# Kernel optimization log

Hardware: AMD Instinct MI355X
Metric: run time of the kernel (lower is better)

The kernel has to match this reference:

```python
import jax, jax.numpy as jnp
import numpy as np

# ---- static configuration (mirrors EarthSpecificBlock/EarthAttention3D) ----
WS = (2, 6, 12)                 # window_size (Z, H, W)
DIM = 192
HEADS = 6
DEPTH = 2
B, Z, H, W = 1, 8, 91, 180      # token grid entering the layer
PAD_H = (WS[1] - H % WS[1]) % WS[1]   # 5
PAD_W = (WS[2] - W % WS[2]) % WS[2]   # 0
HP, WP = H + PAD_H, W + PAD_W         # 96, 180
TOK = WS[0] * WS[1] * WS[2]           # 144 tokens per window
NZ, NH, NW = Z // WS[0], HP // WS[1], WP // WS[2]   # 4, 16, 15
TYPE_W = NZ * NH                      # 64 window types (Z x lat)
BIAS_ROWS = (2 * WS[2] - 1) * WS[1] * WS[1] * WS[0] * WS[0]  # 3312


def _construct_index():
    """Position index into the earth-specific bias table (EarthAttention3D._construct_index)."""
    zi = np.arange(WS[0]); zj = -np.arange(WS[0]) * WS[0]
    hi = np.arange(WS[1]); hj = -np.arange(WS[1]) * WS[1]
    w = np.arange(WS[2])
    c1 = np.stack(np.meshgrid(zi, hi, w, indexing='ij')).reshape(3, -1)
    c2 = np.stack(np.meshgrid(zj, hj, w, indexing='ij')).reshape(3, -1)
    coords = (c1[:, :, None] - c2[:, None, :]).transpose(1, 2, 0)
    coords[:, :, 2] += WS[2] - 1
    coords[:, :, 1] *= 2 * WS[2] - 1
    coords[:, :, 0] *= (2 * WS[2] - 1) * WS[1] * WS[1]
    return coords.sum(-1).reshape(-1)   # (TOK*TOK,)


def _gen_mask():
    """Shifted-window attention mask (gen_mask), shape (1, NW, TYPE_W, 1, TOK, TOK)."""
    m = np.zeros((1, Z, HP, WP, 1), np.float32)
    zs = (slice(0, -WS[0]), slice(-WS[0], -WS[0] // 2), slice(-WS[0] // 2, None))
    hs = (slice(0, -WS[1]), slice(-WS[1], -WS[1] // 2), slice(-WS[1] // 2, None))
    cnt = 0
    for zsl in zs:
        for hsl in hs:
            m[:, zsl, hsl, :, :] = cnt
            cnt += 1
    mw = m.reshape(1, NZ, WS[0], NH, WS[1], NW, WS[2], 1).transpose(0, 1, 3, 5, 2, 4, 6, 7)
    mw = mw.reshape(1, NZ, NH, NW, TOK)
    am = mw[:, :, :, :, None, :] - mw[:, :, :, :, :, None]
    am = np.where(am != 0, np.float32(-100.0), np.float32(0.0))
    return am.transpose(0, 3, 1, 2, 4, 5).reshape(1, NW, TYPE_W, 1, TOK, TOK)


POS_IDX = jnp.asarray(_construct_index())
MASK = jnp.asarray(_gen_mask())


def _ln(x, g, b):
    m = x.mean(-1, keepdims=True)
    v = ((x - m) ** 2).mean(-1, keepdims=True)
    return (x - m) * jax.lax.rsqrt(v + 1e-5) * g + b


def _block(x, qkv_w, qkv_b, proj_w, proj_b, bias_tab, g1, b1, g2, b2, w1, bm1, w2, bm2, roll):
    shortcut = x
    x = jnp.pad(x, ((0, 0), (0, 0), (0, PAD_H), (0, PAD_W), (0, 0)))
    if roll:
        x = jnp.roll(x, (-(WS[0] // 2), -(WS[1] // 2), -(WS[2] // 2)), axis=(1, 2, 3))
    # window partition: (B, NW, TYPE_W, TOK, C)
    xw = x.reshape(B, NZ, WS[0], NH, WS[1], NW, WS[2], DIM).transpose(0, 5, 1, 3, 2, 4, 6, 7)
    xw = xw.reshape(B, NW, TYPE_W, TOK, DIM)
    dh = DIM // HEADS
    qkv = (xw @ qkv_w + qkv_b).reshape(B, NW, TYPE_W, TOK, 3, HEADS, dh)
    qkv = qkv.transpose(4, 0, 1, 2, 5, 3, 6)   # (3, B, NW, TYPE_W, HEADS, TOK, dh)
    q, k, v = qkv[0], qkv[1], qkv[2]
    q = q * (dh ** -0.5)
    attn = jnp.einsum('bwphid,bwphjd->bwphij', q, k)
    bias = bias_tab[POS_IDX].reshape(TOK, TOK, TYPE_W, HEADS).transpose(2, 3, 0, 1)
    attn = attn + bias
    if roll:
        attn = attn + MASK
    attn = jax.nn.softmax(attn, axis=-1)
    out = jnp.einsum('bwphij,bwphjd->bwphid', attn, v)
    out = out.transpose(0, 1, 2, 4, 3, 5).reshape(B, NW, TYPE_W, TOK, DIM)
    out = out @ proj_w + proj_b
    # window merge back to (B, Z, HP, WP, C)
    x = out.reshape(B, NW, NZ, NH, WS[0], WS[1], WS[2], DIM).transpose(0, 2, 4, 3, 5, 1, 6, 7)
    x = x.reshape(B, Z, HP, WP, DIM)
    if roll:
        x = jnp.roll(x, (WS[0] // 2, WS[1] // 2, WS[2] // 2), axis=(1, 2, 3))
    x = x[:, :, :H, :W]
    x = shortcut + _ln(x, g1, b1)           # post-norm residual, as in source
    h = jax.nn.gelu(x @ w1 + bm1, approximate=False)
    h = h @ w2 + bm2
    return x + _ln(h, g2, b2)


def setup_inputs() -> dict:
    key = jax.random.key(0)
    ks = jax.random.split(key, 8)
    s = 0.02
    return {
        'x': jax.random.normal(ks[0], (B, Z, H, W, DIM), jnp.float32),
        'qkv_w': jax.random.normal(ks[1], (DEPTH, DIM, 3 * DIM), jnp.float32) * s,
        'qkv_b': jnp.zeros((DEPTH, 3 * DIM), jnp.float32),
        'proj_w': jax.random.normal(ks[2], (DEPTH, DIM, DIM), jnp.float32) * s,
        'proj_b': jnp.zeros((DEPTH, DIM), jnp.float32),
        'bias_tab': jax.random.normal(ks[3], (DEPTH, BIAS_ROWS, TYPE_W, HEADS), jnp.float32) * s,
        'norm1_g': jnp.ones((DEPTH, DIM), jnp.float32),
        'norm1_b': jnp.zeros((DEPTH, DIM), jnp.float32),
        'norm2_g': jnp.ones((DEPTH, DIM), jnp.float32),
        'norm2_b': jnp.zeros((DEPTH, DIM), jnp.float32),
        'mlp_w1': jax.random.normal(ks[4], (DEPTH, DIM, 4 * DIM), jnp.float32) * s,
        'mlp_b1': jnp.zeros((DEPTH, 4 * DIM), jnp.float32),
        'mlp_w2': jax.random.normal(ks[5], (DEPTH, 4 * DIM, DIM), jnp.float32) * s,
        'mlp_b2': jnp.zeros((DEPTH, DIM), jnp.float32),
    }


def reference(x, qkv_w, qkv_b, proj_w, proj_b, bias_tab, norm1_g, norm1_b,
              norm2_g, norm2_b, mlp_w1, mlp_b1, mlp_w2, mlp_b2):
    for i in range(DEPTH):
        x = _block(x, qkv_w[i], qkv_b[i], proj_w[i], proj_b[i], bias_tab[i],
                   norm1_g[i], norm1_b[i], norm2_g[i], norm2_b[i],
                   mlp_w1[i], mlp_b1[i], mlp_w2[i], mlp_b2[i], roll=(i % 2 == 1))
    return x
```

## Files before the change

kernel.cpp:

```cpp
#include <hip/hip_runtime.h>
#include <math.h>

#define NTOK   131040
#define NTOKW  138240

typedef __attribute__((ext_vector_type(8))) short bf16x8;
typedef __attribute__((ext_vector_type(8))) unsigned short u16x8;
typedef __attribute__((ext_vector_type(4))) float f32x4;

__device__ __forceinline__ float b2f(unsigned short u){
  union { unsigned u; float f; } v; v.u = ((unsigned)u) << 16; return v.f;
}
__device__ __forceinline__ unsigned short f2b(float f){
  union { float f; unsigned u; } v; v.f = f;
  unsigned r = v.u + 0x7FFFu + ((v.u >> 16) & 1u);
  return (unsigned short)(r >> 16);
}
__device__ __forceinline__ float gelu_tanh(float x){
  float t = 0.79788456080286536f * (x + 0.044715f * x * x * x);
  float e = __expf(2.0f * t);
  float th = 1.0f - 2.0f / (e + 1.0f);
  return 0.5f * x * (1.0f + th);
}
__device__ __forceinline__ void lds_barrier(){
  asm volatile("s_waitcnt lgkmcnt(0)" ::: "memory");
  __builtin_amdgcn_sched_barrier(0);
  __builtin_amdgcn_s_barrier();
  __builtin_amdgcn_sched_barrier(0);
}

__global__ __launch_bounds__(256) void transp(const float* __restrict__ src,
                                              unsigned short* __restrict__ dst,
                                              int K, int N){
  int i = blockIdx.x*256 + threadIdx.x;
  if (i < K*N){
    int n = i / K, k = i % K;
    dst[i] = f2b(src[(size_t)k*N + n]);
  }
}

__global__ __launch_bounds__(256) void bias_pre(
    const float* __restrict__ btab,
    unsigned short* __restrict__ bw,
    int roll)
{
  int gid = blockIdx.x*256 + threadIdx.x;
  int pair = gid / 20736;
  int rem  = gid % 20736;
  int i = rem / 144, j = rem % 144;
  int tw = pair / 6, head = pair % 6;
  int ia = i/72, ib = (i%72)/12, ic = i%12;
  int ja = j/72, jb = (j%72)/12, jc = j%12;
  int idx = (ia + 2*ja)*828 + (ib + 6*jb)*23 + (ic - jc + 11);
  float v = btab[(size_t)idx*384 + tw*6 + head];
  if (roll){
    int nz = tw >> 4, nh = tw & 15;
    int zi = nz*2+ia, hi = nh*6+ib, zj = nz*2+ja, hj = nh*6+jb;
    int ri = 3*((zi<6)?0:((zi<7)?1:2)) + ((hi<90)?0:((hi<93)?1:2));
    int rj = 3*((zj<6)?0:((zj<7)?1:2)) + ((hj<90)?0:((hj<93)?1:2));
    if (ri != rj) v -= 100.0f;
  }
  bw[gid] = f2b(v);
}

__global__ __launch_bounds__(256) void gather_win(const float* __restrict__ x,
                                                  unsigned short* __restrict__ xw,
                                                  int roll){
  int gid = blockIdx.x*256 + threadIdx.x;
  int row = gid / 24;
  int dp  = gid % 24;
  int tok = row % 144;
  int wt  = row / 144;
  int tw  = wt & 63;
  int w   = wt >> 6;
  int nz = tw >> 4, nh = tw & 15;
  int wz = tok / 72; int rem = tok % 72; int wh = rem / 12; int ww = rem % 12;
  int z = nz*2 + wz, h = nh*6 + wh, wc = w*12 + ww;
  if (roll){ z = (z+1)&7; h = (h+3)%96; wc = (wc+6)%180; }
  int d0 = dp*8;
  u16x8 o;
  if (h < 91){
    const float* s = x + ((size_t)((z*91 + h)*180 + wc))*192 + d0;
    #pragma unroll
    for (int i=0;i<8;i++) o[i] = f2b(s[i]);
  } else {
    #pragma unroll
    for (int i=0;i<8;i++) o[i] = 0;
  }
  *(u16x8*)(xw + (size_t)row*192 + d0) = o;
}

__global__ __launch_bounds__(512) void gemm_k192(
    const unsigned short* __restrict__ A,
    const unsigned short* __restrict__ Bt,
    const float* __restrict__ bias,
    unsigned short* __restrict__ C,
    int N)
{
  __shared__ unsigned short Bst[192][200];
  int m0 = blockIdx.x * 128;
  int n0 = blockIdx.y * 192;
  int t = threadIdx.x;
  int lane = t & 63, w = t >> 6;
  int wm = w >> 2, wn = w & 3;
  int lg = lane >> 4, lr = lane & 15;

  #pragma unroll
  for (int i=0;i<9;i++){
    int idx = t + i*512;
    int r = idx / 24, c = (idx % 24)*8;
    *(u16x8*)&Bst[r][c] = *(const u16x8*)(Bt + (size_t)(n0 + r)*192 + c);
  }
  __syncthreads();

  const unsigned short* aRow = A + (size_t)(m0 + wm*64 + lr)*192 + lg*8;

  f32x4 acc[4][3];
  #pragma unroll
  for (int a=0;a<4;a++)
    #pragma unroll
    for (int b=0;b<3;b++) acc[a][b] = (f32x4){0.f,0.f,0.f,0.f};

  bf16x8 aP[2][6];
  #pragma unroll
  for (int ks=0; ks<6; ks++) aP[0][ks] = *(const bf16x8*)(aRow + ks*32);

  #pragma unroll
  for (int rt=0; rt<4; rt++){
    if (rt < 3){
      const unsigned short* an = aRow + (size_t)(rt+1)*16*192;
      #pragma unroll
      for (int ks=0; ks<6; ks++) aP[(rt+1)&1][ks] = *(const bf16x8*)(an + ks*32);
    }
    #pragma unroll
    for (int ks=0; ks<6; ks++){
      bf16x8 b0 = *(const bf16x8*)&Bst[wn*48 +      lr][ks*32 + lg*8];
      bf16x8 b1 = *(const bf16x8*)&Bst[wn*48 + 16 + lr][ks*32 + lg*8];
      bf16x8 b2 = *(const bf16x8*)&Bst[wn*48 + 32 + lr][ks*32 + lg*8];
      bf16x8 af = aP[rt&1][ks];
      acc[rt][0] = __builtin_amdgcn_mfma_f32_16x16x32_bf16(af, b0, acc[rt][0], 0,0,0);
      acc[rt][1] = __builtin_amdgcn_mfma_f32_16x16x32_bf16(af, b1, acc[rt][1], 0,0,0);
      acc[rt][2] = __builtin_amdgcn_mfma_f32_16x16x32_bf16(af, b2, acc[rt][2], 0,0,0);
    }
  }

  #pragma unroll
  for (int rt=0; rt<4; rt++){
    #pragma unroll
    for (int fn=0; fn<3; fn++){
      int colg = n0 + wn*48 + fn*16 + lr;
      float bv = bias[colg];
      #pragma unroll
      for (int r=0;r<4;r++){
        int rowg = m0 + wm*64 + rt*16 + lg*4 + r;
        C[(size_t)rowg*N + colg] = f2b(acc[rt][fn][r] + bv);
      }
    }
  }
}

__global__ __launch_bounds__(576) void attn_win(
    const unsigned short* __restrict__ qkv,
    const unsigned short* __restrict__ bw,
    unsigned short* __restrict__ outp)
{
  __shared__ union {
    struct { unsigned short Qs[144][32]; unsigned short Ks[144][40]; } qk;
    unsigned short Ps[144][160];
  } U;
  __shared__ unsigned short Vst[32][160];

  int b = blockIdx.x;
  int head = b % 6;
  int wt = b / 6;
  int tw = wt & 63;
  int t = threadIdx.x;
  int lane = t & 63;
  int wv = t >> 6;
  int lg = lane >> 4, lr = lane & 15;

  {
    int tok = t >> 2, c0 = (t & 3)*8;
    size_t base = ((size_t)wt*144 + tok)*576 + head*32 + c0;
    u16x8 qv = *(const u16x8*)(qkv + base);
    u16x8 kv = *(const u16x8*)(qkv + base + 192);
    u16x8 vv = *(const u16x8*)(qkv + base + 384);
    u16x8 qs;
    #pragma unroll
    for (int i=0;i<8;i++) qs[i] = f2b(b2f(qv[i]) * 0.17677669529663687f);
    *(u16x8*)&U.qk.Qs[tok][c0] = qs;
    *(u16x8*)&U.qk.Ks[tok][c0] = kv;
    #pragma unroll
    for (int i=0;i<8;i++) Vst[c0+i][tok] = vv[i];
  }
  if (t < 512) Vst[t >> 4][144 + (t & 15)] = 0;
  __syncthreads();

  float s[9][4];
  {
    bf16x8 a = *(const bf16x8*)&U.qk.Qs[wv*16 + lr][lg*8];
    #pragma unroll
    for (int ct=0; ct<9; ct++){
      bf16x8 bb = *(const bf16x8*)&U.qk.Ks[ct*16 + lr][lg*8];
      f32x4 d = {0.f,0.f,0.f,0.f};
      d = __builtin_amdgcn_mfma_f32_16x16x32_bf16(a, bb, d, 0,0,0);
      s[ct][0]=d[0]; s[ct][1]=d[1]; s[ct][2]=d[2]; s[ct][3]=d[3];
    }
  }

  {
    const unsigned short* bp = bw + (size_t)(tw*6 + head)*20736;
    int i0 = wv*16 + lg*4;
    #pragma unroll
    for (int ct=0; ct<9; ct++){
      int j = ct*16 + lr;
      #pragma unroll
      for (int r=0;r<4;r++)
        s[ct][r] += b2f(bp[(i0 + r)*144 + j]);
    }
  }

  float mx[4] = {-1e30f,-1e30f,-1e30f,-1e30f};
  #pragma unroll
  for (int ct=0; ct<9; ct++)
    #pragma unroll
    for (int r=0;r<4;r++) mx[r] = fmaxf(mx[r], s[ct][r]);
  #pragma unroll
  for (int off=1; off<16; off<<=1)
    #pragma unroll
    for (int r=0;r<4;r++) mx[r] = fmaxf(mx[r], __shfl_xor(mx[r], off));
  float sm[4] = {0.f,0.f,0.f,0.f};
  #pragma unroll
  for (int ct=0; ct<9; ct++)
    #pragma unroll
    for (int r=0;r<4;r++){ s[ct][r] = __expf(s[ct][r] - mx[r]); sm[r] += s[ct][r]; }
  #pragma unroll
  for (int off=1; off<16; off<<=1)
    #pragma unroll
    for (int r=0;r<4;r++) sm[r] += __shfl_xor(sm[r], off);
  float inv[4];
  #pragma unroll
  for (int r=0;r<4;r++) inv[r] = 1.0f / sm[r];

  lds_barrier();

  #pragma unroll
  for (int ct=0; ct<9; ct++)
    #pragma unroll
    for (int r=0;r<4;r++)
      U.Ps[wv*16 + lg*4 + r][ct*16 + lr] = f2b(s[ct][r] * inv[r]);
  #pragma unroll
  for (int r=0;r<4;r++) U.Ps[wv*16 + lg*4 + r][144 + lr] = 0;
  __syncthreads();

  #pragma unroll
  for (int ct2=0; ct2<2; ct2++){
    f32x4 o = {0.f,0.f,0.f,0.f};
    #pragma unroll
    for (int kt=0; kt<5; kt++){
      bf16x8 a  = *(const bf16x8*)&U.Ps[wv*16 + lr][kt*32 + lg*8];
      bf16x8 bb = *(const bf16x8*)&Vst[ct2*16 + lr][kt*32 + lg*8];
      o = __builtin_amdgcn_mfma_f32_16x16x32_bf16(a, bb, o, 0,0,0);
    }
    size_t rb = ((size_t)wt*144 + wv*16 + lg*4)*192 + head*32 + ct2*16 + lr;
    #pragma unroll
    for (int r=0;r<4;r++) outp[rb + (size_t)r*192] = f2b(o[r]);
  }
}

__global__ __launch_bounds__(256) void unwin_ln(
  const unsigned short* __restrict__ ywin,
  const float* __restrict__ xsrc,
  const float* __restrict__ g, const float* __restrict__ bb,
  float* __restrict__ outf, unsigned short* __restrict__ outb, int roll)
{
  int tok = blockIdx.x*4 + (threadIdx.x>>6);
  if (tok >= NTOK) return;
  int lane = threadIdx.x & 63;
  int z = tok / (91*180);
  int rem = tok % (91*180);
  int h = rem / 180, wc = rem % 180;
  int zz=z, hh=h, ww=wc;
  if (roll){ zz = (z+7)&7; hh = (h+93)%96; ww = (wc+174)%180; }
  int nz = zz>>1, wz = zz&1;
  int nh = hh/6,  wh = hh%6;
  int nw = ww/12, w2 = ww%12;
  size_t row = ((size_t)(nw*64 + nz*16 + nh))*144 + wz*72 + wh*12 + w2;
  const unsigned short* yr = ywin + row*192;
  float v[3]; float s=0.f, ss=0.f;
  #pragma unroll
  for (int i=0;i<3;i++){ v[i] = b2f(yr[lane + i*64]); s += v[i]; ss += v[i]*v[i]; }
  #pragma unroll
  for (int off=32; off>=1; off>>=1){ s += __shfl_xor(s, off); ss += __shfl_xor(ss, off); }
  float mean = s * (1.0f/192.0f);
  float var = ss * (1.0f/192.0f) - mean*mean;
  float rinv = rsqrtf(var + 1e-5f);
  size_t tb = (size_t)tok*192;
  #pragma unroll
  for (int i=0;i<3;i++){
    int d = lane + i*64;
    float o = xsrc[tb + d] + ((v[i]-mean)*rinv*g[d] + bb[d]);
    outf[tb+d] = o;
    outb[tb+d] = f2b(o);
  }
}

__global__ __launch_bounds__(512) void mlp_fused(
    const unsigned short* __restrict__ A,
    const unsigned short* __restrict__ W1t,
    const float* __restrict__ bias1,
    const unsigned short* __restrict__ W2t,
    const float* __restrict__ bias2,
    unsigned short* __restrict__ C,
    int M)
{
  __shared__ unsigned short W1s[32][200];
  __shared__ unsigned short W2s[192][40];
  __shared__ unsigned short Hs[8][16][40];
  __shared__ float b1s[768];
  int m0 = blockIdx.x*128;
  int t = threadIdx.x, lane = t & 63, w = t >> 6;
  int lg = lane >> 4, lr = lane & 15;

  int arow = m0 + w*16 + lr;
  bf16x8 afr[6];
  if (arow < M){
    const unsigned short* ap = A + (size_t)arow*192 + lg*8;
    #pragma unroll
    for (int ks=0; ks<6; ks++) afr[ks] = *(const bf16x8*)(ap + ks*32);
  } else {
    #pragma unroll
    for (int ks=0; ks<6; ks++)
      #pragma unroll
      for (int j=0;j<8;j++) afr[ks][j] = 0;
  }

  b1s[t < 768 ? t : 0] = bias1[t < 768 ? t : 0];
  if (t < 256) b1s[512 + t] = bias1[512 + t];

  int i1r[2], i1c[2], i2r[2], i2c[2];
  #pragma unroll
  for (int i=0;i<2;i++){
    int idx = t + i*512;
    i1r[i] = idx/24; i1c[i] = (idx%24)*8;
    i2r[i] = idx/4;  i2c[i] = (idx&3)*8;
  }
  bool g2nd = (t + 512) < 768;

  u16x8 w1r[2], w2r[2];
  w1r[0] = *(const u16x8*)(W1t + (size_t)i1r[0]*192 + i1c[0]);
  w2r[0] = *(const u16x8*)(W2t + (size_t)i2r[0]*768 + i2c[0]);
  if (g2nd){
    w1r[1] = *(const u16x8*)(W1t + (size_t)i1r[1]*192 + i1c[1]);
    w2r[1] = *(const u16x8*)(W2t + (size_t)i2r[1]*768 + i2c[1]);
  }

  f32x4 acc[12];
  #pragma unroll
  for (int i=0;i<12;i++) acc[i] = (f32x4){0.f,0.f,0.f,0.f};

  for (int it=0; it<24; ++it){
    int hc = it*32;
    *(u16x8*)&W1s[i1r[0]][i1c[0]] = w1r[0];
    *(u16x8*)&W2s[i2r[0]][i2c[0]] = w2r[0];
    if (g2nd){
      *(u16x8*)&W1s[i1r[1]][i1c[1]] = w1r[1];
      *(u16x8*)&W2s[i2r[1]][i2c[1]] = w2r[1];
    }
    if (it < 23){
      int hc2 = hc + 32;
      w1r[0] = *(const u16x8*)(W1t + (size_t)(hc2 + i1r[0])*192 + i1c[0]);
      w2r[0] = *(const u16x8*)(W2t + (size_t)i2r[0]*768 + hc2 + i2c[0]);
      if (g2nd){
        w1r[1] = *(const u16x8*)(W1t + (size_t)(hc2 + i1r[1])*192 + i1c[1]);
        w2r[1] = *(const u16x8*)(W2t + (size_t)i2r[1]*768 + hc2 + i2c[1]);
      }
    }
    lds_barrier();

    f32x4 h0 = (f32x4){0.f,0.f,0.f,0.f};
    f32x4 h1 = (f32x4){0.f,0.f,0.f,0.f};
    #pragma unroll
    for (int ks=0; ks<6; ks++){
      bf16x8 b0 = *(const bf16x8*)&W1s[lr][ks*32 + lg*8];
      bf16x8 b1f = *(const bf16x8*)&W1s[16 + lr][ks*32 + lg*8];
      h0 = __builtin_amdgcn_mfma_f32_16x16x32_bf16(afr[ks], b0, h0, 0,0,0);
      h1 = __builtin_amdgcn_mfma_f32_16x16x32_bf16(afr[ks], b1f, h1, 0,0,0);
    }
    float bb0 = b1s[hc + lr];
    float bb1 = b1s[hc + 16 + lr];
    #pragma unroll
    for (int r=0;r<4;r++){
      Hs[w][lg*4 + r][lr]      = f2b(gelu_tanh(h0[r] + bb0));
      Hs[w][lg*4 + r][16 + lr] = f2b(gelu_tanh(h1[r] + bb1));
    }
    bf16x8 pa = *(const bf16x8*)&Hs[w][lr][lg*8];
    #pragma unroll
    for (int fn=0; fn<12; fn++){
      bf16x8 bb = *(const bf16x8*)&W2s[fn*16 + lr][lg*8];
      acc[fn] = __builtin_amdgcn_mfma_f32_16x16x32_bf16(pa, bb, acc[fn], 0,0,0);
    }
    lds_barrier();
  }

  #pragma unroll
  for (int fn=0; fn<12; fn++){
    float b2v = bias2[fn*16 + lr];
    #pragma unroll
    for (int r=0;r<4;r++){
      int crow = m0 + w*16 + lg*4 + r;
      if (crow < M) C[(size_t)crow*192 + fn*16 + lr] = f2b(acc[fn][r] + b2v);
    }
  }
}

__global__ __launch_bounds__(256) void add_ln(
  const unsigned short* __restrict__ ymlp,
  const float* __restrict__ xmid,
  const float* __restrict__ g, const float* __restrict__ bb,
  float* __restrict__ outf)
{
  int tok = blockIdx.x*4 + (threadIdx.x>>6);
  if (tok >= NTOK) return;
  int lane = threadIdx.x & 63;
  const unsigned short* yr = ymlp + (size_t)tok*192;
  float v[3]; float s=0.f, ss=0.f;
  #pragma unroll
  for (int i=0;i<3;i++){ v[i] = b2f(yr[lane + i*64]); s += v[i]; ss += v[i]*v[i]; }
  #pragma unroll
  for (int off=32; off>=1; off>>=1){ s += __shfl_xor(s, off); ss += __shfl_xor(ss, off); }
  float mean = s * (1.0f/192.0f);
  float var = ss * (1.0f/192.0f) - mean*mean;
  float rinv = rsqrtf(var + 1e-5f);
  size_t tb = (size_t)tok*192;
  #pragma unroll
  for (int i=0;i<3;i++){
    int d = lane + i*64;
    outf[tb+d] = xmid[tb + d] + ((v[i]-mean)*rinv*g[d] + bb[d]);
  }
}

extern "C" void kernel_launch(void* const* d_in, const int* in_sizes, int n_in,
                              void* d_out, int out_size, void* d_ws, size_t ws_size,
                              hipStream_t stream)
{
  const float* x_in    = (const float*)d_in[0];
  const float* qkvw    = (const float*)d_in[1];
  const float* qkvbias = (const float*)d_in[2];
  const float* projw   = (const float*)d_in[3];
  const float* projbias= (const float*)d_in[4];
  const float* btab    = (const float*)d_in[5];
  const float* n1g = (const float*)d_in[6];
  const float* n1b = (const float*)d_in[7];
  const float* n2g = (const float*)d_in[8];
  const float* n2b = (const float*)d_in[9];
  const float* w1  = (const float*)d_in[10];
  const float* b1  = (const float*)d_in[11];
  const float* w2  = (const float*)d_in[12];
  const float* b2  = (const float*)d_in[13];
  float* outp = (float*)d_out;

  const size_t REG_A = (size_t)NTOKW*192;
  const size_t REG_B = (size_t)NTOKW*576;
  const size_t W_QT  = (size_t)2*576*192;
  const size_t W_PT  = (size_t)2*192*192;
  const size_t W_1T  = (size_t)2*768*192;
  const size_t W_2T  = (size_t)2*192*768;
  const size_t TOT_SH = REG_A + REG_B + W_QT + W_PT + W_1T + W_2T;
  const size_t NEEDED = TOT_SH*2 + (size_t)NTOK*192*4;
  if (ws_size < NEEDED) return;

  unsigned short* ws16 = (unsigned short*)d_ws;
  size_t off = 0;
  unsigned short* regA = ws16 + off; off += REG_A;
  unsigned short* regB = ws16 + off; off += REG_B;
  unsigned short* wqt  = ws16 + off; off += W_QT;
  unsigned short* wpt  = ws16 + off; off += W_PT;
  unsigned short* w1t  = ws16 + off; off += W_1T;
  unsigned short* w2t  = ws16 + off; off += W_2T;
  float* xmidf = (float*)(ws16 + off);
  unsigned short* bw = (unsigned short*)xmidf;

  for (int dep=0; dep<2; dep++){
    transp<<<(192*576+255)/256,256,0,stream>>>(qkvw + (size_t)dep*192*576,
                                               wqt + (size_t)dep*576*192, 192, 576);
    transp<<<(192*192+255)/256,256,0,stream>>>(projw + (size_t)dep*192*192,
                                               wpt + (size_t)dep*192*192, 192, 192);
    transp<<<(192*768+255)/256,256,0,stream>>>(w1 + (size_t)dep*192*768,
                                               w1t + (size_t)dep*768*192, 192, 768);
    transp<<<(768*192+255)/256,256,0,stream>>>(w2 + (size_t)dep*768*192,
                                               w2t + (size_t)dep*192*768, 768, 192);
  }

  for (int dep=0; dep<2; dep++){
    int roll = dep;
    const float* xs = (dep==0) ? x_in : outp;
    float* xout = outp;

    gather_win<<<NTOKW*24/256, 256, 0, stream>>>(xs, regA, roll);

    dim3 g1(NTOKW/128, 3);
    gemm_k192<<<g1, 512, 0, stream>>>(regA, wqt + (size_t)dep*576*192,
                                      qkvbias + dep*576, regB, 576);

    bias_pre<<<(64*6*20736)/256, 256, 0, stream>>>(btab + (size_t)dep*3312*384, bw, roll);

    attn_win<<<960*6, 576, 0, stream>>>(regB, bw, regA);

    dim3 g2(NTOKW/128, 1);
    gemm_k192<<<g2, 512, 0, stream>>>(regA, wpt + (size_t)dep*192*192,
                                      projbias + dep*192, regB, 192);

    unwin_ln<<<NTOK/4, 256, 0, stream>>>(regB, xs, n1g + dep*192, n1b + dep*192,
                                         xmidf, regA, roll);

    mlp_fused<<<(NTOK+127)/128, 512, 0, stream>>>(regA, w1t + (size_t)dep*768*192,
                                                  b1 + dep*768, w2t + (size_t)dep*192*768,
                                                  b2 + dep*192, regB, NTOK);

    add_ln<<<NTOK/4, 256, 0, stream>>>(regB, xmidf, n2g + dep*192, n2b + dep*192, xout);
  }
}
```

Measured before the change: 1.159 ms.

## Fuse residual add and LayerNorm into MLP epilogue, use sigmoid GELU and packed stores

New measurement: 1.155 ms. No clear change (-0.4%).

```diff
diff --git a/kernel.cpp b/kernel.cpp
--- a/kernel.cpp
+++ b/kernel.cpp
@@ -7,6 +7,7 @@
 typedef __attribute__((ext_vector_type(8))) short bf16x8;
 typedef __attribute__((ext_vector_type(8))) unsigned short u16x8;
 typedef __attribute__((ext_vector_type(4))) float f32x4;
+typedef __attribute__((ext_vector_type(2))) float f32x2;
 
 __device__ __forceinline__ float b2f(unsigned short u){
   union { unsigned u; float f; } v; v.u = ((unsigned)u) << 16; return v.f;
@@ -16,11 +17,14 @@
   unsigned r = v.u + 0x7FFFu + ((v.u >> 16) & 1u);
   return (unsigned short)(r >> 16);
 }
-__device__ __forceinline__ float gelu_tanh(float x){
-  float t = 0.79788456080286536f * (x + 0.044715f * x * x * x);
-  float e = __expf(2.0f * t);
-  float th = 1.0f - 2.0f / (e + 1.0f);
-  return 0.5f * x * (1.0f + th);
+__device__ __forceinline__ float gelu_sig(float x){
+  float e = __expf(-1.702f * x);
+  return x * __builtin_amdgcn_rcpf(1.0f + e);
+}
+__device__ __forceinline__ unsigned pk_bf16(float lo, float hi){
+  unsigned r;
+  asm("v_cvt_pk_bf16_f32 %0, %1, %2" : "=v"(r) : "v"(lo), "v"(hi));
+  return r;
 }
 __device__ __forceinline__ void lds_barrier(){
   asm volatile("s_waitcnt lgkmcnt(0)" ::: "memory");
@@ -305,19 +309,23 @@
   }
 }
 
-__global__ __launch_bounds__(512) void mlp_fused(
+__global__ __launch_bounds__(512) void mlp_fused_ln(
     const unsigned short* __restrict__ A,
     const unsigned short* __restrict__ W1t,
     const float* __restrict__ bias1,
     const unsigned short* __restrict__ W2t,
-    const float* __restrict__ bias2,
-    unsigned short* __restrict__ C,
+    const float* __restrict__ mbias2,
+    const float* __restrict__ xmid,
+    const float* __restrict__ lng,
+    const float* __restrict__ lnb,
+    float* __restrict__ outF,
     int M)
 {
-  __shared__ unsigned short W1s[32][200];
-  __shared__ unsigned short W2s[192][40];
+  __shared__ unsigned short W1s[32][196];
+  __shared__ unsigned short W2s[192][44];
   __shared__ unsigned short Hs[8][16][40];
   __shared__ float b1s[768];
+  __shared__ float eps[576];
   int m0 = blockIdx.x*128;
   int t = threadIdx.x, lane = t & 63, w = t >> 6;
   int lg = lane >> 4, lr = lane & 15;
@@ -335,8 +343,9 @@
       for (int j=0;j<8;j++) afr[ks][j] = 0;
   }
 
-  b1s[t < 768 ? t : 0] = bias1[t < 768 ? t : 0];
+  b1s[t] = bias1[t];
   if (t < 256) b1s[512 + t] = bias1[512 + t];
+  if (t < 192){ eps[t] = mbias2[t]; eps[192 + t] = lng[t]; eps[384 + t] = lnb[t]; }
 
   int i1r[2], i1c[2], i2r[2], i2c[2];
   #pragma unroll
@@ -382,61 +391,58 @@
     f32x4 h1 = (f32x4){0.f,0.f,0.f,0.f};
     #pragma unroll
     for (int ks=0; ks<6; ks++){
-      bf16x8 b0 = *(const bf16x8*)&W1s[lr][ks*32 + lg*8];
-      bf16x8 b1f = *(const bf16x8*)&W1s[16 + lr][ks*32 + lg*8];
+      bf16x8 b0  = *(const bf16x8*)&W1s[2*lr    ][ks*32 + lg*8];
+      bf16x8 b1f = *(const bf16x8*)&W1s[2*lr + 1][ks*32 + lg*8];
       h0 = __builtin_amdgcn_mfma_f32_16x16x32_bf16(afr[ks], b0, h0, 0,0,0);
       h1 = __builtin_amdgcn_mfma_f32_16x16x32_bf16(afr[ks], b1f, h1, 0,0,0);
     }
-    float bb0 = b1s[hc + lr];
-    float bb1 = b1s[hc + 16 + lr];
+    float bb0 = b1s[hc + 2*lr];
+    float bb1 = b1s[hc + 2*lr + 1];
     #pragma unroll
     for (int r=0;r<4;r++){
-      Hs[w][lg*4 + r][lr]      = f2b(gelu_tanh(h0[r] + bb0));
-      Hs[w][lg*4 + r][16 + lr] = f2b(gelu_tanh(h1[r] + bb1));
+      unsigned pk = pk_bf16(gelu_sig(h0[r] + bb0), gelu_sig(h1[r] + bb1));
+      *(unsigned*)&Hs[w][lg*4 + r][2*lr] = pk;
     }
     bf16x8 pa = *(const bf16x8*)&Hs[w][lr][lg*8];
     #pragma unroll
-    for (int fn=0; fn<12; fn++){
-      bf16x8 bb = *(const bf16x8*)&W2s[fn*16 + lr][lg*8];
-      acc[fn] = __builtin_amdgcn_mfma_f32_16x16x32_bf16(pa, bb, acc[fn], 0,0,0);
+    for (int f=0; f<6; f++){
+      bf16x8 c0 = *(const bf16x8*)&W2s[f*32 + 2*lr    ][lg*8];
+      bf16x8 c1 = *(const bf16x8*)&W2s[f*32 + 2*lr + 1][lg*8];
+      acc[2*f]   = __builtin_amdgcn_mfma_f32_16x16x32_bf16(pa, c0, acc[2*f],   0,0,0);
+      acc[2*f+1] = __builtin_amdgcn_mfma_f32_16x16x32_bf16(pa, c1, acc[2*f+1], 0,0,0);
     }
     lds_barrier();
   }
 
   #pragma unroll
-  for (int fn=0; fn<12; fn++){
-    float b2v = bias2[fn*16 + lr];
-    #pragma unroll
-    for (int r=0;r<4;r++){
-      int crow = m0 + w*16 + lg*4 + r;
-      if (crow < M) C[(size_t)crow*192 + fn*16 + lr] = f2b(acc[fn][r] + b2v);
-    }
-  }
-}
-
-__global__ __launch_bounds__(256) void add_ln(
-  const unsigned short* __restrict__ ymlp,
-  const float* __restrict__ xmid,
-  const float* __restrict__ g, const float* __restrict__ bb,
-  float* __restrict__ outf)
-{
-  int tok = blockIdx.x*4 + (threadIdx.x>>6);
-  if (tok >= NTOK) return;
-  int lane = threadIdx.x & 63;
-  const unsigned short* yr = ymlp + (size_t)tok*192;
-  float v[3]; float s=0.f, ss=0.f;
-  #pragma unroll
-  for (int i=0;i<3;i++){ v[i] = b2f(yr[lane + i*64]); s += v[i]; ss += v[i]*v[i]; }
-  #pragma unroll
-  for (int off=32; off>=1; off>>=1){ s += __shfl_xor(s, off); ss += __shfl_xor(ss, off); }
-  float mean = s * (1.0f/192.0f);
-  float var = ss * (1.0f/192.0f) - mean*mean;
-  float rinv = rsqrtf(var + 1e-5f);
-  size_t tb = (size_t)tok*192;
-  #pragma unroll
-  for (int i=0;i<3;i++){
-    int d = lane + i*64;
-    outf[tb+d] = xmid[tb + d] + ((v[i]-mean)*rinv*g[d] + bb[d]);
+  for (int r=0;r<4;r++){
+    int row = m0 + w*16 + lg*4 + r;
+    float s = 0.f, ss = 0.f;
+    #pragma unroll
+    for (int f=0; f<6; f++){
+      float v0 = acc[2*f][r]   + eps[f*32 + 2*lr];
+      float v1 = acc[2*f+1][r] + eps[f*32 + 2*lr + 1];
+      s += v0 + v1; ss += v0*v0 + v1*v1;
+    }
+    #pragma unroll
+    for (int off=1; off<16; off<<=1){ s += __shfl_xor(s, off); ss += __shfl_xor(ss, off); }
+    float mean = s * (1.0f/192.0f);
+    float var  = ss * (1.0f/192.0f) - mean*mean;
+    float rinv = rsqrtf(var + 1e-5f);
+    if (row < M){
+      size_t base = (size_t)row*192;
+      #pragma unroll
+      for (int f=0; f<6; f++){
+        int c0 = f*32 + 2*lr;
+        float v0 = acc[2*f][r]   + eps[c0];
+        float v1 = acc[2*f+1][r] + eps[c0 + 1];
+        f32x2 xm = *(const f32x2*)&xmid[base + c0];
+        f32x2 o;
+        o[0] = xm[0] + (v0 - mean)*rinv*eps[192 + c0]     + eps[384 + c0];
+        o[1] = xm[1] + (v1 - mean)*rinv*eps[192 + c0 + 1] + eps[384 + c0 + 1];
+        *(f32x2*)&outF[base + c0] = o;
+      }
+    }
   }
 }
 
@@ -514,10 +520,9 @@
     unwin_ln<<<NTOK/4, 256, 0, stream>>>(regB, xs, n1g + dep*192, n1b + dep*192,
                                          xmidf, regA, roll);
 
-    mlp_fused<<<(NTOK+127)/128, 512, 0, stream>>>(regA, w1t + (size_t)dep*768*192,
-                                                  b1 + dep*768, w2t + (size_t)dep*192*768,
-                                                  b2 + dep*192, regB, NTOK);
-
-    add_ln<<<NTOK/4, 256, 0, stream>>>(regB, xmidf, n2g + dep*192, n2b + dep*192, xout);
-  }
-}
+    mlp_fused_ln<<<(NTOK+127)/128, 512, 0, stream>>>(
+        regA, w1t + (size_t)dep*768*192, b1 + dep*768,
+        w2t + (size_t)dep*192*768, b2 + dep*192,
+        xmidf, n2g + dep*192, n2b + dep*192, xout, NTOK);
+  }
+}
```
